# Performance work log

Measured on AMD Instinct MI355X. Metric: run time of the kernel, lower is better.

The kernel has to match this reference:

```python
import jax, jax.numpy as jnp
import numpy as np

ALPHA = 0.2          # LeakyReLU negative slope
NEG_BIG = -9e15      # mask value from original code


def setup_inputs() -> dict:
    key = jax.random.key(0)
    k1, k2, k3, k4 = jax.random.split(key, 4)
    B, N, F_in, F_out = 16, 1024, 256, 256
    x = jax.random.normal(k1, (B, N, F_in), dtype=jnp.float32)
    adj = jax.random.randint(k2, (B, N, N), 0, 2, dtype=jnp.int32)
    # xavier-uniform-like scales
    W = jax.random.normal(k3, (F_in, F_out), dtype=jnp.float32) * np.sqrt(2.0 / (F_in + F_out))
    a = jax.random.normal(k4, (2 * F_out, 1), dtype=jnp.float32) * np.sqrt(2.0 / (2 * F_out + 1))
    return {"x": x, "adj": adj, "W": W, "a": a}


def reference(x, adj, W, a):
    # x: [B,N,Fin], adj: [B,N,N] (int mask), W: [Fin,Fout], a: [2*Fout,1]
    F_out = a.shape[0] // 2
    h = jnp.einsum("bni,io->bno", x, W)            # [B,N,Fout]
    # Decompose a into left/right halves: e_ij = lrelu(a_l.h_i + a_r.h_j)
    a_l = a[:F_out, 0]                               # [Fout]
    a_r = a[F_out:, 0]                               # [Fout]
    el = h @ a_l                                     # [B,N] score contribution of target i
    er = h @ a_r                                     # [B,N] score contribution of source j
    e = jax.nn.leaky_relu(el[:, :, None] + er[:, None, :], ALPHA)  # [B,N,N]
    e = jnp.where(adj > 0, e, NEG_BIG)
    attn = jax.nn.softmax(e, axis=-1)                # masked softmax over neighbors j
    # weighted sum of neighbor features; concat with n_heads=1 is identity
    return jnp.einsum("bij,bjo->bio", attn, h)       # [B,N,Fout]
```

## Files before the change

### kernel.cpp

```cpp
#include <hip/hip_runtime.h>
#include <stdint.h>

#define ALPHA 0.2f
#define NEG_BIG -9000000000000000.0f

typedef __attribute__((ext_vector_type(8))) short bf16x8;
typedef __attribute__((ext_vector_type(8))) unsigned short u16x8;
typedef __attribute__((ext_vector_type(4))) float f32x4;

__device__ __forceinline__ unsigned short f2bf(float f) {
    unsigned int u = __float_as_uint(f);
    u += 0x7fffu + ((u >> 16) & 1u);
    return (unsigned short)(u >> 16);
}

__device__ __forceinline__ void gload_lds16(const void* g, void* l) {
    __builtin_amdgcn_global_load_lds(
        (const __attribute__((address_space(1))) unsigned int*)g,
        (__attribute__((address_space(3))) unsigned int*)l, 16, 0, 0);
}

__global__ void wt_wa_kernel(const float* __restrict__ W,
                             const float* __restrict__ a,
                             unsigned short* __restrict__ Wtbf,
                             float* __restrict__ wa) {
    const int t = threadIdx.x;
    if (blockIdx.x < 256) {
        const int o = blockIdx.x;
        Wtbf[o * 256 + t] = f2bf(W[t * 256 + o]);
    } else {
        float sl = 0.f, sr = 0.f;
        const float* wr = W + t * 256;
        for (int o = 0; o < 256; ++o) {
            const float wv = wr[o];
            sl += wv * a[o];
            sr += wv * a[256 + o];
        }
        wa[t] = sl;
        wa[256 + t] = sr;
    }
}

__global__ __launch_bounds__(256) void eler2x_kernel(
    const float* __restrict__ x, const float* __restrict__ wa,
    float* __restrict__ el, float* __restrict__ er,
    unsigned short* __restrict__ xbf)
{
    const int w = threadIdx.x >> 6, l = threadIdx.x & 63;
    const int r = blockIdx.x * 4 + w;
    const float4 xv = *(const float4*)(x + (size_t)r * 256 + l * 4);
    const float4 al = *(const float4*)(wa + l * 4);
    const float4 ar = *(const float4*)(wa + 256 + l * 4);

    ushort4 xb;
    xb.x = f2bf(xv.x); xb.y = f2bf(xv.y); xb.z = f2bf(xv.z); xb.w = f2bf(xv.w);
    *(ushort4*)(xbf + (size_t)r * 256 + l * 4) = xb;

    float sl = xv.x * al.x + xv.y * al.y + xv.z * al.z + xv.w * al.w;
    float sr = xv.x * ar.x + xv.y * ar.y + xv.z * ar.z + xv.w * ar.w;
#pragma unroll
    for (int off = 32; off >= 1; off >>= 1) {
        sl += __shfl_xor(sl, off);
        sr += __shfl_xor(sr, off);
    }
    if (l == 0) { el[r] = sl; er[r] = sr; }
}

__global__ __launch_bounds__(256) void gemm_h(
    const unsigned short* __restrict__ A,
    const unsigned short* __restrict__ Bt,
    unsigned short* __restrict__ C)
{
    __shared__ __align__(16) unsigned short As[64 * 64];
    __shared__ __align__(16) unsigned short Bs[128 * 64];

    const int tid = threadIdx.x;
    const int w = tid >> 6, l = tid & 63;
    const int q = l >> 4, ml = l & 15;
    const int wm = (w >> 1) * 32;
    const int wn = (w & 1) * 64;
    const int m0 = blockIdx.y * 64;
    const int n0 = blockIdx.x * 128;

    f32x4 acc[2][4];
    for (int i = 0; i < 2; ++i)
        for (int j = 0; j < 4; ++j) {
            f32x4 z = {0.f, 0.f, 0.f, 0.f};
            acc[i][j] = z;
        }

    for (int k0 = 0; k0 < 256; k0 += 64) {
        for (int c = 0; c < 2; ++c) {
            const int cb = c * 256 + (w << 6);
            const int p = cb + l;
            const int r = p >> 3;
            const int cc = (p & 7) ^ (r & 7);
            gload_lds16(A + (size_t)(m0 + r) * 256 + k0 + cc * 8, As + cb * 8);
        }
        for (int c = 0; c < 4; ++c) {
            const int cb = c * 256 + (w << 6);
            const int p = cb + l;
            const int r = p >> 3;
            const int cc = (p & 7) ^ (r & 7);
            gload_lds16(Bt + (size_t)(n0 + r) * 256 + k0 + cc * 8, Bs + cb * 8);
        }
        __syncthreads();

        bf16x8 aF[2][2], bF[2][4];
#pragma unroll
        for (int ks = 0; ks < 2; ++ks) {
#pragma unroll
            for (int mt = 0; mt < 2; ++mt) {
                const int mm = wm + mt * 16 + ml;
                aF[ks][mt] = *(const bf16x8*)(As + (mm * 8 + ((ks * 4 + q) ^ (mm & 7))) * 8);
            }
#pragma unroll
            for (int nt = 0; nt < 4; ++nt) {
                const int nn = wn + nt * 16 + ml;
                bF[ks][nt] = *(const bf16x8*)(Bs + (nn * 8 + ((ks * 4 + q) ^ (nn & 7))) * 8);
            }
        }
#pragma unroll
        for (int ks = 0; ks < 2; ++ks)
            for (int mt = 0; mt < 2; ++mt)
                for (int nt = 0; nt < 4; ++nt)
                    acc[mt][nt] = __builtin_amdgcn_mfma_f32_16x16x32_bf16(
                        aF[ks][mt], bF[ks][nt], acc[mt][nt], 0, 0, 0);
        __syncthreads();
    }

    for (int mt = 0; mt < 2; ++mt)
        for (int nt = 0; nt < 4; ++nt) {
            const int gn = n0 + wn + nt * 16 + ml;
            for (int r = 0; r < 4; ++r) {
                const int gm = m0 + wm + mt * 16 + q * 4 + r;
                C[(size_t)gm * 16384 + gn] = f2bf(acc[mt][nt][r]);
            }
        }
}

__global__ __launch_bounds__(256) void mask_kernel(
    const int* __restrict__ adj,
    const float* __restrict__ el,
    const float* __restrict__ er,
    float* __restrict__ c,
    unsigned short* __restrict__ pk16)
{
    __shared__ unsigned char nibs[4][256];

    const int w = threadIdx.x >> 6, l = threadIdx.x & 63;
    const int row = blockIdx.x * 4 + w;
    const int b = row >> 10;
    const int* arow = adj + (size_t)row * 1024;
    const float* erb = er + (b << 10);
    const float eli = el[row];

    float ev[16];
    float m = -3.0e38f;
#pragma unroll
    for (int it = 0; it < 4; ++it) {
        const int j = it * 256 + l * 4;
        const int4 av = *(const int4*)(arow + j);
        const float4 erv = *(const float4*)(erb + j);
        float e0 = eli + erv.x; e0 = e0 > 0.f ? e0 : ALPHA * e0; e0 = av.x > 0 ? e0 : NEG_BIG;
        float e1 = eli + erv.y; e1 = e1 > 0.f ? e1 : ALPHA * e1; e1 = av.y > 0 ? e1 : NEG_BIG;
        float e2 = eli + erv.z; e2 = e2 > 0.f ? e2 : ALPHA * e2; e2 = av.z > 0 ? e2 : NEG_BIG;
        float e3 = eli + erv.w; e3 = e3 > 0.f ? e3 : ALPHA * e3; e3 = av.w > 0 ? e3 : NEG_BIG;
        ev[it * 4 + 0] = e0; ev[it * 4 + 1] = e1;
        ev[it * 4 + 2] = e2; ev[it * 4 + 3] = e3;
        m = fmaxf(m, fmaxf(fmaxf(e0, e1), fmaxf(e2, e3)));
        nibs[w][it * 64 + l] =
            (unsigned char)((av.x > 0) | ((av.y > 0) << 1) |
                            ((av.z > 0) << 2) | ((av.w > 0) << 3));
    }
#pragma unroll
    for (int off = 32; off >= 1; off >>= 1) m = fmaxf(m, __shfl_xor(m, off));
    float s = 0.f;
#pragma unroll
    for (int u = 0; u < 16; ++u) s += __expf(ev[u] - m);
#pragma unroll
    for (int off = 32; off >= 1; off >>= 1) s += __shfl_xor(s, off);
    if (l == 0) c[row] = m + __logf(s);

    const unsigned nr = *(const unsigned int*)(&nibs[w][l * 4]);
    const unsigned short mask16 =
        (unsigned short)((nr & 0xFu) | ((nr >> 4) & 0xF0u) |
                         ((nr >> 8) & 0xF00u) | ((nr >> 12) & 0xF000u));
    pk16[(size_t)row * 64 + l] = mask16;
}

__global__ __launch_bounds__(256) void pv_kernel(
    const unsigned short* __restrict__ pk16,
    const float* __restrict__ el,
    const float* __restrict__ er,
    const float* __restrict__ c,
    const unsigned short* __restrict__ hT,
    float* __restrict__ out)
{
    __shared__ float er_s[1024];
    __shared__ __align__(16) unsigned short pk_s[32 * 64];
    __shared__ __align__(16) unsigned short Hs[256 * 64];
    __shared__ __align__(16) unsigned short Ps[32 * 72];

    const int tid = threadIdx.x;
    const int w = tid >> 6, l = tid & 63;
    const int q = l >> 4, ml = l & 15;
    const int b = blockIdx.y;
    const int i0 = blockIdx.x * 32;

    *(float4*)(er_s + tid * 4) = *(const float4*)(er + (b << 10) + tid * 4);
    *(u16x8*)(pk_s + tid * 8) =
        *(const u16x8*)(pk16 + ((size_t)(b << 10) + i0) * 64 + tid * 8);
    const int ib = tid >> 3;
    const int js = (tid & 7) * 8;
    const float eli_b = el[(b << 10) + i0 + ib];
    const float ci = c[(b << 10) + i0 + ib];
    __syncthreads();

    f32x4 acc[2][4];
    for (int i = 0; i < 2; ++i)
        for (int j = 0; j < 4; ++j) {
            f32x4 z = {0.f, 0.f, 0.f, 0.f};
            acc[i][j] = z;
        }

    const unsigned short* hb = hT + (size_t)b * 1024;

    for (int j0 = 0; j0 < 1024; j0 += 64) {
        for (int cr = 0; cr < 8; ++cr) {
            const int cb = cr * 256 + (w << 6);
            const int p = cb + l;
            const int r = p >> 3;
            const int cc = (p & 7) ^ (r & 7);
            gload_lds16(hb + (size_t)r * 16384 + j0 + cc * 8, Hs + cb * 8);
        }
        {
            const unsigned hw = pk_s[ib * 64 + ((j0 + js) >> 4)];
            const unsigned v = (hw >> ((j0 + js) & 15)) & 0xFFu;
            u16x8 pvv;
#pragma unroll
            for (int u = 0; u < 8; ++u) {
                float e = eli_b + er_s[j0 + js + u];
                e = e > 0.f ? e : ALPHA * e;
                const float p = ((v >> u) & 1u) ? __expf(e - ci) : 0.f;
                pvv[u] = f2bf(p);
            }
            *(u16x8*)(Ps + ib * 72 + js) = pvv;
        }
        __syncthreads();

        bf16x8 aF[2][2], bF[2][4];
#pragma unroll
        for (int ks = 0; ks < 2; ++ks) {
#pragma unroll
            for (int mt = 0; mt < 2; ++mt)
                aF[ks][mt] = *(const bf16x8*)(Ps + (mt * 16 + ml) * 72 + ks * 32 + q * 8);
#pragma unroll
            for (int nt = 0; nt < 4; ++nt) {
                const int oc = (w << 6) + nt * 16 + ml;
                bF[ks][nt] = *(const bf16x8*)(Hs + (oc * 8 + ((ks * 4 + q) ^ (oc & 7))) * 8);
            }
        }
#pragma unroll
        for (int ks = 0; ks < 2; ++ks)
            for (int mt = 0; mt < 2; ++mt)
                for (int nt = 0; nt < 4; ++nt)
                    acc[mt][nt] = __builtin_amdgcn_mfma_f32_16x16x32_bf16(
                        aF[ks][mt], bF[ks][nt], acc[mt][nt], 0, 0, 0);
        __syncthreads();
    }

    float* ob = out + (size_t)b * 262144;
    for (int mt = 0; mt < 2; ++mt)
        for (int nt = 0; nt < 4; ++nt) {
            const int gn = (w << 6) + nt * 16 + ml;
            for (int r = 0; r < 4; ++r) {
                const int gm = i0 + mt * 16 + q * 4 + r;
                ob[(size_t)gm * 256 + gn] = acc[mt][nt][r];
            }
        }
}

extern "C" void kernel_launch(void* const* d_in, const int* in_sizes, int n_in,
                              void* d_out, int out_size, void* d_ws, size_t ws_size,
                              hipStream_t stream) {
    const float* x   = (const float*)d_in[0];
    const int*   adj = (const int*)d_in[1];
    const float* W   = (const float*)d_in[2];
    const float* a   = (const float*)d_in[3];
    float* out = (float*)d_out;

    char* ws = (char*)d_ws;
    unsigned short* Wtbf  = (unsigned short*)(ws);
    float* wa             = (float*)(ws + 131072);
    unsigned short* xbf   = (unsigned short*)(ws + 133120);
    unsigned short* h_T   = (unsigned short*)(ws + 8521728);
    float* el             = (float*)(ws + 16910336);
    float* er             = (float*)(ws + 16975872);
    float* c              = (float*)(ws + 17041408);
    unsigned short* pk16  = (unsigned short*)(ws + 17106944);

    wt_wa_kernel<<<dim3(257), dim3(256), 0, stream>>>(W, a, Wtbf, wa);

    eler2x_kernel<<<dim3(4096), dim3(256), 0, stream>>>(x, wa, el, er, xbf);

    gemm_h<<<dim3(128, 4), dim3(256), 0, stream>>>(Wtbf, xbf, h_T);

    mask_kernel<<<dim3(4096), dim3(256), 0, stream>>>(adj, el, er, c, pk16);

    pv_kernel<<<dim3(32, 16), dim3(256), 0, stream>>>(pk16, el, er, c, h_T, out);
}
```

Before: 155.1 us.

## Merge h GEMM and adjacency mask kernels into one interleaved launch

The bf16 GEMM that produces h^T and the adjacency mask/logsumexp kernel become a single launch of 4608 blocks. Every eighth block among the first 4096 does a GEMM tile and the rest do mask rows, so the compute-bound GEMM overlaps with the bandwidth-bound adj scan. This removes one launch and the serialization between two independent stages. In exchange the merged kernel's LDS footprint is the union of both (about 25 KB per block), which may lower occupancy for the mask blocks.

```diff
diff --git a/kernel.cpp b/kernel.cpp
--- a/kernel.cpp
+++ b/kernel.cpp
@@ -66,127 +66,128 @@
     if (l == 0) { el[r] = sl; er[r] = sr; }
 }
 
-__global__ __launch_bounds__(256) void gemm_h(
+__global__ __launch_bounds__(256) void gemm_mask_kernel(
     const unsigned short* __restrict__ A,
     const unsigned short* __restrict__ Bt,
-    unsigned short* __restrict__ C)
-{
-    __shared__ __align__(16) unsigned short As[64 * 64];
-    __shared__ __align__(16) unsigned short Bs[128 * 64];
-
-    const int tid = threadIdx.x;
-    const int w = tid >> 6, l = tid & 63;
-    const int q = l >> 4, ml = l & 15;
-    const int wm = (w >> 1) * 32;
-    const int wn = (w & 1) * 64;
-    const int m0 = blockIdx.y * 64;
-    const int n0 = blockIdx.x * 128;
-
-    f32x4 acc[2][4];
-    for (int i = 0; i < 2; ++i)
-        for (int j = 0; j < 4; ++j) {
-            f32x4 z = {0.f, 0.f, 0.f, 0.f};
-            acc[i][j] = z;
-        }
-
-    for (int k0 = 0; k0 < 256; k0 += 64) {
-        for (int c = 0; c < 2; ++c) {
-            const int cb = c * 256 + (w << 6);
-            const int p = cb + l;
-            const int r = p >> 3;
-            const int cc = (p & 7) ^ (r & 7);
-            gload_lds16(A + (size_t)(m0 + r) * 256 + k0 + cc * 8, As + cb * 8);
-        }
-        for (int c = 0; c < 4; ++c) {
-            const int cb = c * 256 + (w << 6);
-            const int p = cb + l;
-            const int r = p >> 3;
-            const int cc = (p & 7) ^ (r & 7);
-            gload_lds16(Bt + (size_t)(n0 + r) * 256 + k0 + cc * 8, Bs + cb * 8);
-        }
-        __syncthreads();
-
-        bf16x8 aF[2][2], bF[2][4];
-#pragma unroll
-        for (int ks = 0; ks < 2; ++ks) {
-#pragma unroll
-            for (int mt = 0; mt < 2; ++mt) {
-                const int mm = wm + mt * 16 + ml;
-                aF[ks][mt] = *(const bf16x8*)(As + (mm * 8 + ((ks * 4 + q) ^ (mm & 7))) * 8);
-            }
-#pragma unroll
-            for (int nt = 0; nt < 4; ++nt) {
-                const int nn = wn + nt * 16 + ml;
-                bF[ks][nt] = *(const bf16x8*)(Bs + (nn * 8 + ((ks * 4 + q) ^ (nn & 7))) * 8);
-            }
-        }
-#pragma unroll
-        for (int ks = 0; ks < 2; ++ks)
-            for (int mt = 0; mt < 2; ++mt)
-                for (int nt = 0; nt < 4; ++nt)
-                    acc[mt][nt] = __builtin_amdgcn_mfma_f32_16x16x32_bf16(
-                        aF[ks][mt], bF[ks][nt], acc[mt][nt], 0, 0, 0);
-        __syncthreads();
-    }
-
-    for (int mt = 0; mt < 2; ++mt)
-        for (int nt = 0; nt < 4; ++nt) {
-            const int gn = n0 + wn + nt * 16 + ml;
-            for (int r = 0; r < 4; ++r) {
-                const int gm = m0 + wm + mt * 16 + q * 4 + r;
-                C[(size_t)gm * 16384 + gn] = f2bf(acc[mt][nt][r]);
-            }
-        }
-}
-
-__global__ __launch_bounds__(256) void mask_kernel(
+    unsigned short* __restrict__ C,
     const int* __restrict__ adj,
     const float* __restrict__ el,
     const float* __restrict__ er,
     float* __restrict__ c,
     unsigned short* __restrict__ pk16)
 {
+    __shared__ __align__(16) unsigned short As[64 * 64];
+    __shared__ __align__(16) unsigned short Bs[128 * 64];
     __shared__ unsigned char nibs[4][256];
 
-    const int w = threadIdx.x >> 6, l = threadIdx.x & 63;
-    const int row = blockIdx.x * 4 + w;
-    const int b = row >> 10;
-    const int* arow = adj + (size_t)row * 1024;
-    const float* erb = er + (b << 10);
-    const float eli = el[row];
-
-    float ev[16];
-    float m = -3.0e38f;
-#pragma unroll
-    for (int it = 0; it < 4; ++it) {
-        const int j = it * 256 + l * 4;
-        const int4 av = *(const int4*)(arow + j);
-        const float4 erv = *(const float4*)(erb + j);
-        float e0 = eli + erv.x; e0 = e0 > 0.f ? e0 : ALPHA * e0; e0 = av.x > 0 ? e0 : NEG_BIG;
-        float e1 = eli + erv.y; e1 = e1 > 0.f ? e1 : ALPHA * e1; e1 = av.y > 0 ? e1 : NEG_BIG;
-        float e2 = eli + erv.z; e2 = e2 > 0.f ? e2 : ALPHA * e2; e2 = av.z > 0 ? e2 : NEG_BIG;
-        float e3 = eli + erv.w; e3 = e3 > 0.f ? e3 : ALPHA * e3; e3 = av.w > 0 ? e3 : NEG_BIG;
-        ev[it * 4 + 0] = e0; ev[it * 4 + 1] = e1;
-        ev[it * 4 + 2] = e2; ev[it * 4 + 3] = e3;
-        m = fmaxf(m, fmaxf(fmaxf(e0, e1), fmaxf(e2, e3)));
-        nibs[w][it * 64 + l] =
-            (unsigned char)((av.x > 0) | ((av.y > 0) << 1) |
-                            ((av.z > 0) << 2) | ((av.w > 0) << 3));
+    const int id = blockIdx.x;
+    const int tid = threadIdx.x;
+    const int w = tid >> 6, l = tid & 63;
+
+    if (id < 4096 && (id & 7) == 0) {
+        const int gid = id >> 3;
+        const int n0 = (gid & 127) * 128;
+        const int m0 = (gid >> 7) * 64;
+        const int q = l >> 4, ml = l & 15;
+        const int wm = (w >> 1) * 32;
+        const int wn = (w & 1) * 64;
+
+        f32x4 acc[2][4];
+        for (int i = 0; i < 2; ++i)
+            for (int j = 0; j < 4; ++j) {
+                f32x4 z = {0.f, 0.f, 0.f, 0.f};
+                acc[i][j] = z;
+            }
+
+        for (int k0 = 0; k0 < 256; k0 += 64) {
+            for (int cc2 = 0; cc2 < 2; ++cc2) {
+                const int cb = cc2 * 256 + (w << 6);
+                const int p = cb + l;
+                const int r = p >> 3;
+                const int cc = (p & 7) ^ (r & 7);
+                gload_lds16(A + (size_t)(m0 + r) * 256 + k0 + cc * 8, As + cb * 8);
+            }
+            for (int cc2 = 0; cc2 < 4; ++cc2) {
+                const int cb = cc2 * 256 + (w << 6);
+                const int p = cb + l;
+                const int r = p >> 3;
+                const int cc = (p & 7) ^ (r & 7);
+                gload_lds16(Bt + (size_t)(n0 + r) * 256 + k0 + cc * 8, Bs + cb * 8);
+            }
+            __syncthreads();
+
+            bf16x8 aF[2][2], bF[2][4];
+#pragma unroll
+            for (int ks = 0; ks < 2; ++ks) {
+#pragma unroll
+                for (int mt = 0; mt < 2; ++mt) {
+                    const int mm = wm + mt * 16 + ml;
+                    aF[ks][mt] = *(const bf16x8*)(As + (mm * 8 + ((ks * 4 + q) ^ (mm & 7))) * 8);
+                }
+#pragma unroll
+                for (int nt = 0; nt < 4; ++nt) {
+                    const int nn = wn + nt * 16 + ml;
+                    bF[ks][nt] = *(const bf16x8*)(Bs + (nn * 8 + ((ks * 4 + q) ^ (nn & 7))) * 8);
+                }
+            }
+#pragma unroll
+            for (int ks = 0; ks < 2; ++ks)
+                for (int mt = 0; mt < 2; ++mt)
+                    for (int nt = 0; nt < 4; ++nt)
+                        acc[mt][nt] = __builtin_amdgcn_mfma_f32_16x16x32_bf16(
+                            aF[ks][mt], bF[ks][nt], acc[mt][nt], 0, 0, 0);
+            __syncthreads();
+        }
+
+        for (int mt = 0; mt < 2; ++mt)
+            for (int nt = 0; nt < 4; ++nt) {
+                const int gn = n0 + wn + nt * 16 + ml;
+                for (int r = 0; r < 4; ++r) {
+                    const int gm = m0 + wm + mt * 16 + q * 4 + r;
+                    C[(size_t)gm * 16384 + gn] = f2bf(acc[mt][nt][r]);
+                }
+            }
+    } else {
+        const int mblk = (id < 4096) ? (id - (id >> 3) - 1) : (3584 + (id - 4096));
+        const int row = mblk * 4 + w;
+        const int b = row >> 10;
+        const int* arow = adj + (size_t)row * 1024;
+        const float* erb = er + (b << 10);
+        const float eli = el[row];
+
+        float ev[16];
+        float m = -3.0e38f;
+#pragma unroll
+        for (int it = 0; it < 4; ++it) {
+            const int j = it * 256 + l * 4;
+            const int4 av = *(const int4*)(arow + j);
+            const float4 erv = *(const float4*)(erb + j);
+            float e0 = eli + erv.x; e0 = e0 > 0.f ? e0 : ALPHA * e0; e0 = av.x > 0 ? e0 : NEG_BIG;
+            float e1 = eli + erv.y; e1 = e1 > 0.f ? e1 : ALPHA * e1; e1 = av.y > 0 ? e1 : NEG_BIG;
+            float e2 = eli + erv.z; e2 = e2 > 0.f ? e2 : ALPHA * e2; e2 = av.z > 0 ? e2 : NEG_BIG;
+            float e3 = eli + erv.w; e3 = e3 > 0.f ? e3 : ALPHA * e3; e3 = av.w > 0 ? e3 : NEG_BIG;
+            ev[it * 4 + 0] = e0; ev[it * 4 + 1] = e1;
+            ev[it * 4 + 2] = e2; ev[it * 4 + 3] = e3;
+            m = fmaxf(m, fmaxf(fmaxf(e0, e1), fmaxf(e2, e3)));
+            nibs[w][it * 64 + l] =
+                (unsigned char)((av.x > 0) | ((av.y > 0) << 1) |
+                                ((av.z > 0) << 2) | ((av.w > 0) << 3));
+        }
+#pragma unroll
+        for (int off = 32; off >= 1; off >>= 1) m = fmaxf(m, __shfl_xor(m, off));
+        float s = 0.f;
+#pragma unroll
+        for (int u = 0; u < 16; ++u) s += __expf(ev[u] - m);
+#pragma unroll
+        for (int off = 32; off >= 1; off >>= 1) s += __shfl_xor(s, off);
+        if (l == 0) c[row] = m + __logf(s);
+
+        const unsigned nr = *(const unsigned int*)(&nibs[w][l * 4]);
+        const unsigned short mask16 =
+            (unsigned short)((nr & 0xFu) | ((nr >> 4) & 0xF0u) |
+                             ((nr >> 8) & 0xF00u) | ((nr >> 12) & 0xF000u));
+        pk16[(size_t)row * 64 + l] = mask16;
     }
-#pragma unroll
-    for (int off = 32; off >= 1; off >>= 1) m = fmaxf(m, __shfl_xor(m, off));
-    float s = 0.f;
-#pragma unroll
-    for (int u = 0; u < 16; ++u) s += __expf(ev[u] - m);
-#pragma unroll
-    for (int off = 32; off >= 1; off >>= 1) s += __shfl_xor(s, off);
-    if (l == 0) c[row] = m + __logf(s);
-
-    const unsigned nr = *(const unsigned int*)(&nibs[w][l * 4]);
-    const unsigned short mask16 =
-        (unsigned short)((nr & 0xFu) | ((nr >> 4) & 0xF0u) |
-                         ((nr >> 8) & 0xF00u) | ((nr >> 12) & 0xF000u));
-    pk16[(size_t)row * 64 + l] = mask16;
 }
 
 __global__ __launch_bounds__(256) void pv_kernel(
@@ -304,9 +305,8 @@
 
     eler2x_kernel<<<dim3(4096), dim3(256), 0, stream>>>(x, wa, el, er, xbf);
 
-    gemm_h<<<dim3(128, 4), dim3(256), 0, stream>>>(Wtbf, xbf, h_T);
-
-    mask_kernel<<<dim3(4096), dim3(256), 0, stream>>>(adj, el, er, c, pk16);
+    gemm_mask_kernel<<<dim3(4608), dim3(256), 0, stream>>>(
+        Wtbf, xbf, h_T, adj, el, er, c, pk16);
 
     pv_kernel<<<dim3(32, 16), dim3(256), 0, stream>>>(pk16, el, er, c, h_T, out);
 }
```

Measured after the change: 173.7 us. +12.0%, slower.
